# Optimization experiments

Hardware: AMD Instinct MI355X
Metric: run time of the kernel (lower is better)

The kernel has to match this reference:

```python
import jax, jax.numpy as jnp
import numpy as np

B, N, C, OUT, K2 = 64, 4096, 64, 64, 4  # batch, lattice sites, in/out features, kersize^2

def setup_inputs() -> dict:
    key = jax.random.key(0)
    k1, k2, k3, k4 = jax.random.split(key, 4)
    std = 0.5 / jnp.sqrt(K2 * (C + OUT))  # matches module's init stddev (W_scale=b_scale=1)
    x = jax.random.normal(k1, (B, N, C), dtype=jnp.float32)
    W = jax.random.normal(k2, (K2, C, OUT), dtype=jnp.float32) * std
    b = jax.random.normal(k3, (OUT,), dtype=jnp.float32) * std
    kernel2 = jax.random.randint(k4, (N, K2), 0, N, dtype=jnp.int32)
    return {"x": x, "W": W, "b": b, "kernel2": kernel2}

def reference(x, W, b, kernel2):
    # gather neighbors: [B, N, K2, C]; contract (K2, C) with W -> [B, N, OUT]
    y = jnp.einsum('bnkc,kco->bno', x[:, kernel2, :], W)
    # bias broadcast (original used tensordot with ones([B,N]))
    return y + b
```

## Files before the change

kernel.cpp:

```cpp
#include <hip/hip_runtime.h>
#include <stdint.h>


#define N_SITES  4096
#define C_DIM    64
#define OUT_DIM  64

typedef __attribute__((ext_vector_type(8))) short bf16x8;
typedef __attribute__((ext_vector_type(4))) float f32x4;

__device__ __forceinline__ uint32_t pack2_bf16(float f0, float f1) {
    uint32_t u0 = __float_as_uint(f0) + 0x8000u;
    uint32_t u1 = __float_as_uint(f1) + 0x8000u;
    return __builtin_amdgcn_perm(u1, u0, 0x07060302u);
}

template<int N> __device__ __forceinline__ void wait_vmcnt() {
    asm volatile("s_waitcnt vmcnt(%0)" :: "n"(N) : "memory");
}

__device__ __forceinline__ void gll16(const float* p, uint32_t m0v) {
    asm volatile("s_mov_b32 m0, %1\n\t"
                 "global_load_lds_dwordx4 %0, off"
                 :: "v"(p), "s"(m0v) : "memory");
}

__global__ __launch_bounds__(64, 1)
void conv_async_kernel(const float* __restrict__ x, const float* __restrict__ W,
                       const float* __restrict__ bias, const int* __restrict__ kernel2,
                       float* __restrict__ out)
{
    __shared__ __align__(16) uint8_t lds_raw[33792];

    const int lane = threadIdx.x;
    const int bi   = blockIdx.x;
    const int sg   = bi >> 4;
    const int bg   = bi & 15;
    const int n0   = sg * 64;
    const int b0   = bg * 4;

    const int c  = lane & 15;
    const int q  = lane >> 4;
    const int sl = c >> 2;
    const int bb = c & 3;

    {
        int4 iv = ((const int4*)kernel2)[n0 + lane];
        *(int4*)(lds_raw + 32768 + lane * 16) = iv;
    }

    bf16x8 aw[4][8];
    #pragma unroll
    for (int t = 0; t < 4; ++t)
        #pragma unroll
        for (int s = 0; s < 8; ++s) {
            uint32_t* ap = (uint32_t*)&aw[t][s];
            #pragma unroll
            for (int u = 0; u < 4; ++u) {
                float f0 = W[(size_t)(s*32 + q*8 + 2*u    ) * OUT_DIM + t*16 + c];
                float f1 = W[(size_t)(s*32 + q*8 + 2*u + 1) * OUT_DIM + t*16 + c];
                ap[u] = pack2_bf16(f0, f1);
            }
        }

    f32x4 bias_r[4];
    #pragma unroll
    for (int t = 0; t < 4; ++t) bias_r[t] = *(const f32x4*)&bias[t*16 + q*4];

    const float* gx = x + (size_t)(b0 + bb) * (N_SITES * C_DIM) + q * 4;

    const uint32_t lds0 =
        __builtin_amdgcn_readfirstlane((uint32_t)(uintptr_t)lds_raw);

    wait_vmcnt<0>();

    auto issue_tile = [&](int pp) {
        const uint8_t* ib = lds_raw + 32768 + pp * 64;
        int4 iv0 = *(const int4*)(ib);
        int4 iv1 = *(const int4*)(ib + 16);
        int4 iv2 = *(const int4*)(ib + 32);
        int4 iv3 = *(const int4*)(ib + 48);
        const uint32_t m0b = lds0 + (uint32_t)(pp & 1) * 16384;
        #pragma unroll
        for (int ks = 0; ks < 4; ++ks) {
            const int e0 = ks==0 ? iv0.x : ks==1 ? iv0.y : ks==2 ? iv0.z : iv0.w;
            const int e1 = ks==0 ? iv1.x : ks==1 ? iv1.y : ks==2 ? iv1.z : iv1.w;
            const int e2 = ks==0 ? iv2.x : ks==1 ? iv2.y : ks==2 ? iv2.z : iv2.w;
            const int e3 = ks==0 ? iv3.x : ks==1 ? iv3.y : ks==2 ? iv3.z : iv3.w;
            const int nk = (sl & 2) ? ((sl & 1) ? e3 : e2)
                                    : ((sl & 1) ? e1 : e0);
            const float* row = gx + (size_t)(uint32_t)nk * C_DIM;
            gll16(row,      m0b + (uint32_t)(ks*4 + 0) * 1024);
            gll16(row + 16, m0b + (uint32_t)(ks*4 + 1) * 1024);
            gll16(row + 32, m0b + (uint32_t)(ks*4 + 2) * 1024);
            gll16(row + 48, m0b + (uint32_t)(ks*4 + 3) * 1024);
        }
    };

    issue_tile(0);
    issue_tile(1);

    #pragma unroll
    for (int p = 0; p < 16; ++p) {
        if      (p == 0)  wait_vmcnt<16>();
        else if (p == 1)  wait_vmcnt<20>();
        else if (p == 15) wait_vmcnt<8>();
        else              wait_vmcnt<24>();

        const uint32_t tb = (uint32_t)(p & 1) * 16384;
        f32x4 acc[4];
        #pragma unroll
        for (int t = 0; t < 4; ++t) acc[t] = (f32x4){0.f, 0.f, 0.f, 0.f};

        #pragma unroll
        for (int s = 0; s < 8; ++s) {
            const uint8_t* pb = lds_raw + tb + s*2048 + q*512 + c*16;
            f32x4 xa = *(const f32x4*)(pb);
            f32x4 xb = *(const f32x4*)(pb + 256);
            bf16x8 bf;
            uint32_t* bp = (uint32_t*)&bf;
            bp[0] = pack2_bf16(xa[0], xa[1]);
            bp[1] = pack2_bf16(xa[2], xa[3]);
            bp[2] = pack2_bf16(xb[0], xb[1]);
            bp[3] = pack2_bf16(xb[2], xb[3]);
            #pragma unroll
            for (int t = 0; t < 4; ++t)
                acc[t] = __builtin_amdgcn_mfma_f32_16x16x32_bf16(aw[t][s], bf, acc[t], 0, 0, 0);
        }

        if (p + 2 < 16) issue_tile(p + 2);

        const int n = n0 + p*4 + sl;
        float* op = out + ((size_t)(b0 + bb) * N_SITES + n) * OUT_DIM + q*4;
        #pragma unroll
        for (int t = 0; t < 4; ++t)
            *(f32x4*)(op + t*16) = acc[t] + bias_r[t];
    }
}

extern "C" void kernel_launch(void* const* d_in, const int* in_sizes, int n_in,
                              void* d_out, int out_size, void* d_ws, size_t ws_size,
                              hipStream_t stream) {
    const float* x       = (const float*)d_in[0];
    const float* W       = (const float*)d_in[1];
    const float* bias    = (const float*)d_in[2];
    const int*   kernel2 = (const int*)d_in[3];
    float* out = (float*)d_out;

    conv_async_kernel<<<1024, 64, 0, stream>>>(x, W, bias, kernel2, out);
}
```

Measured before the change: 144.7 us.

## Halve per-block site tile and pipeline gathers in half-tiles to double grid

```diff
diff --git a/kernel.cpp b/kernel.cpp
--- a/kernel.cpp
+++ b/kernel.cpp
@@ -30,13 +30,13 @@
                        const float* __restrict__ bias, const int* __restrict__ kernel2,
                        float* __restrict__ out)
 {
-    __shared__ __align__(16) uint8_t lds_raw[33792];
+    __shared__ __align__(16) uint8_t lds_raw[16896];
 
     const int lane = threadIdx.x;
     const int bi   = blockIdx.x;
     const int sg   = bi >> 4;
     const int bg   = bi & 15;
-    const int n0   = sg * 64;
+    const int n0   = sg * 32;
     const int b0   = bg * 4;
 
     const int c  = lane & 15;
@@ -44,9 +44,9 @@
     const int sl = c >> 2;
     const int bb = c & 3;
 
-    {
+    if (lane < 32) {
         int4 iv = ((const int4*)kernel2)[n0 + lane];
-        *(int4*)(lds_raw + 32768 + lane * 16) = iv;
+        *(int4*)(lds_raw + 16384 + lane * 16) = iv;
     }
 
     bf16x8 aw[4][8];
@@ -74,46 +74,34 @@
 
     wait_vmcnt<0>();
 
-    auto issue_tile = [&](int pp) {
-        const uint8_t* ib = lds_raw + 32768 + pp * 64;
-        int4 iv0 = *(const int4*)(ib);
-        int4 iv1 = *(const int4*)(ib + 16);
-        int4 iv2 = *(const int4*)(ib + 32);
-        int4 iv3 = *(const int4*)(ib + 48);
-        const uint32_t m0b = lds0 + (uint32_t)(pp & 1) * 16384;
+    auto issue_ht = [&](int i) {
+        const uint8_t* ib = lds_raw + 16384 + (i >> 1) * 64 + (i & 1) * 8;
+        int2 iv0 = *(const int2*)(ib);
+        int2 iv1 = *(const int2*)(ib + 16);
+        int2 iv2 = *(const int2*)(ib + 32);
+        int2 iv3 = *(const int2*)(ib + 48);
+        const uint32_t m0b = lds0 + (uint32_t)(i & 1) * 8192;
         #pragma unroll
-        for (int ks = 0; ks < 4; ++ks) {
-            const int e0 = ks==0 ? iv0.x : ks==1 ? iv0.y : ks==2 ? iv0.z : iv0.w;
-            const int e1 = ks==0 ? iv1.x : ks==1 ? iv1.y : ks==2 ? iv1.z : iv1.w;
-            const int e2 = ks==0 ? iv2.x : ks==1 ? iv2.y : ks==2 ? iv2.z : iv2.w;
-            const int e3 = ks==0 ? iv3.x : ks==1 ? iv3.y : ks==2 ? iv3.z : iv3.w;
+        for (int kl = 0; kl < 2; ++kl) {
+            const int e0 = kl ? iv0.y : iv0.x;
+            const int e1 = kl ? iv1.y : iv1.x;
+            const int e2 = kl ? iv2.y : iv2.x;
+            const int e3 = kl ? iv3.y : iv3.x;
             const int nk = (sl & 2) ? ((sl & 1) ? e3 : e2)
                                     : ((sl & 1) ? e1 : e0);
             const float* row = gx + (size_t)(uint32_t)nk * C_DIM;
-            gll16(row,      m0b + (uint32_t)(ks*4 + 0) * 1024);
-            gll16(row + 16, m0b + (uint32_t)(ks*4 + 1) * 1024);
-            gll16(row + 32, m0b + (uint32_t)(ks*4 + 2) * 1024);
-            gll16(row + 48, m0b + (uint32_t)(ks*4 + 3) * 1024);
+            gll16(row,      m0b + (uint32_t)(kl*4 + 0) * 1024);
+            gll16(row + 16, m0b + (uint32_t)(kl*4 + 1) * 1024);
+            gll16(row + 32, m0b + (uint32_t)(kl*4 + 2) * 1024);
+            gll16(row + 48, m0b + (uint32_t)(kl*4 + 3) * 1024);
         }
     };
 
-    issue_tile(0);
-    issue_tile(1);
-
-    #pragma unroll
-    for (int p = 0; p < 16; ++p) {
-        if      (p == 0)  wait_vmcnt<16>();
-        else if (p == 1)  wait_vmcnt<20>();
-        else if (p == 15) wait_vmcnt<8>();
-        else              wait_vmcnt<24>();
-
-        const uint32_t tb = (uint32_t)(p & 1) * 16384;
-        f32x4 acc[4];
+    auto comp_ht = [&](int i, f32x4* acc) {
+        const uint32_t tb = (uint32_t)(i & 1) * 8192;
+        const int hb = (i & 1) * 4;
         #pragma unroll
-        for (int t = 0; t < 4; ++t) acc[t] = (f32x4){0.f, 0.f, 0.f, 0.f};
-
-        #pragma unroll
-        for (int s = 0; s < 8; ++s) {
+        for (int s = 0; s < 4; ++s) {
             const uint8_t* pb = lds_raw + tb + s*2048 + q*512 + c*16;
             f32x4 xa = *(const f32x4*)(pb);
             f32x4 xb = *(const f32x4*)(pb + 256);
@@ -125,10 +113,29 @@
             bp[3] = pack2_bf16(xb[2], xb[3]);
             #pragma unroll
             for (int t = 0; t < 4; ++t)
-                acc[t] = __builtin_amdgcn_mfma_f32_16x16x32_bf16(aw[t][s], bf, acc[t], 0, 0, 0);
+                acc[t] = __builtin_amdgcn_mfma_f32_16x16x32_bf16(aw[t][hb + s], bf, acc[t], 0, 0, 0);
         }
+    };
 
-        if (p + 2 < 16) issue_tile(p + 2);
+    issue_ht(0);
+    issue_ht(1);
+
+    #pragma unroll
+    for (int p = 0; p < 8; ++p) {
+        f32x4 acc[4];
+        #pragma unroll
+        for (int t = 0; t < 4; ++t) acc[t] = (f32x4){0.f, 0.f, 0.f, 0.f};
+
+        if (p == 0) wait_vmcnt<8>();
+        else        wait_vmcnt<12>();
+        comp_ht(2*p, acc);
+        if (p < 7) issue_ht(2*p + 2);
+
+        if      (p == 0) wait_vmcnt<8>();
+        else if (p == 7) wait_vmcnt<4>();
+        else             wait_vmcnt<12>();
+        comp_ht(2*p + 1, acc);
+        if (p < 7) issue_ht(2*p + 3);
 
         const int n = n0 + p*4 + sl;
         float* op = out + ((size_t)(b0 + bb) * N_SITES + n) * OUT_DIM + q*4;
@@ -147,5 +154,5 @@
     const int*   kernel2 = (const int*)d_in[3];
     float* out = (float*)d_out;
 
-    conv_async_kernel<<<1024, 64, 0, stream>>>(x, W, bias, kernel2, out);
+    conv_async_kernel<<<2048, 64, 0, stream>>>(x, W, bias, kernel2, out);
 }
```

New measurement: 149.8 us. 1.04x slower.

## Gather neighbor rows into registers with triple-buffered loads instead of LDS DMA

Applied to the files above, without the earlier changes.

```diff
diff --git a/kernel.cpp b/kernel.cpp
--- a/kernel.cpp
+++ b/kernel.cpp
@@ -19,24 +19,36 @@
     asm volatile("s_waitcnt vmcnt(%0)" :: "n"(N) : "memory");
 }
 
-__device__ __forceinline__ void gll16(const float* p, uint32_t m0v) {
-    asm volatile("s_mov_b32 m0, %1\n\t"
-                 "global_load_lds_dwordx4 %0, off"
-                 :: "v"(p), "s"(m0v) : "memory");
+template<int OFF>
+__device__ __forceinline__ void gld16(f32x4& d, const float* p) {
+    asm volatile("global_load_dwordx4 %0, %1, off offset:%2"
+                 : "=v"(d) : "v"(p), "n"(OFF) : "memory");
+}
+
+__host__ __device__ constexpr int wait_for(int i) {
+    return (i == 0 || i == 1) ? 16
+         : (i == 2)           ? 20
+         : (i == 14)          ? 16
+         : (i == 15)          ? 4
+         : (i & 1)            ? 20
+         : 24;
 }
 
 __global__ __launch_bounds__(64, 1)
-void conv_async_kernel(const float* __restrict__ x, const float* __restrict__ W,
-                       const float* __restrict__ bias, const int* __restrict__ kernel2,
-                       float* __restrict__ out)
+void conv_vgather_kernel(const float* __restrict__ x, const float* __restrict__ W,
+                         const float* __restrict__ bias, const int* __restrict__ kernel2,
+                         float* __restrict__ out)
 {
-    __shared__ __align__(16) uint8_t lds_raw[33792];
+    __shared__ __align__(16) int lds_idx[32 * 4];
 
     const int lane = threadIdx.x;
     const int bi   = blockIdx.x;
-    const int sg   = bi >> 4;
-    const int bg   = bi & 15;
-    const int n0   = sg * 64;
+    const int half = bi >> 10;
+    const int r    = bi & 1023;
+    const int bgl  = r & 7;
+    const int sg   = r >> 3;
+    const int bg   = bgl + half * 8;
+    const int n0   = sg * 32;
     const int b0   = bg * 4;
 
     const int c  = lane & 15;
@@ -44,10 +56,8 @@
     const int sl = c >> 2;
     const int bb = c & 3;
 
-    {
-        int4 iv = ((const int4*)kernel2)[n0 + lane];
-        *(int4*)(lds_raw + 32768 + lane * 16) = iv;
-    }
+    if (lane < 32)
+        ((int4*)lds_idx)[lane] = ((const int4*)kernel2)[n0 + lane];
 
     bf16x8 aw[4][8];
     #pragma unroll
@@ -67,75 +77,79 @@
     #pragma unroll
     for (int t = 0; t < 4; ++t) bias_r[t] = *(const f32x4*)&bias[t*16 + q*4];
 
-    const float* gx = x + (size_t)(b0 + bb) * (N_SITES * C_DIM) + q * 4;
-
-    const uint32_t lds0 =
-        __builtin_amdgcn_readfirstlane((uint32_t)(uintptr_t)lds_raw);
+    const float* gxb = x + (size_t)(b0 + bb) * (N_SITES * C_DIM) + q * 8;
 
     wait_vmcnt<0>();
+    __builtin_amdgcn_sched_barrier(0);
 
-    auto issue_tile = [&](int pp) {
-        const uint8_t* ib = lds_raw + 32768 + pp * 64;
-        int4 iv0 = *(const int4*)(ib);
-        int4 iv1 = *(const int4*)(ib + 16);
-        int4 iv2 = *(const int4*)(ib + 32);
-        int4 iv3 = *(const int4*)(ib + 48);
-        const uint32_t m0b = lds0 + (uint32_t)(pp & 1) * 16384;
-        #pragma unroll
-        for (int ks = 0; ks < 4; ++ks) {
-            const int e0 = ks==0 ? iv0.x : ks==1 ? iv0.y : ks==2 ? iv0.z : iv0.w;
-            const int e1 = ks==0 ? iv1.x : ks==1 ? iv1.y : ks==2 ? iv1.z : iv1.w;
-            const int e2 = ks==0 ? iv2.x : ks==1 ? iv2.y : ks==2 ? iv2.z : iv2.w;
-            const int e3 = ks==0 ? iv3.x : ks==1 ? iv3.y : ks==2 ? iv3.z : iv3.w;
-            const int nk = (sl & 2) ? ((sl & 1) ? e3 : e2)
-                                    : ((sl & 1) ? e1 : e0);
-            const float* row = gx + (size_t)(uint32_t)nk * C_DIM;
-            gll16(row,      m0b + (uint32_t)(ks*4 + 0) * 1024);
-            gll16(row + 16, m0b + (uint32_t)(ks*4 + 1) * 1024);
-            gll16(row + 32, m0b + (uint32_t)(ks*4 + 2) * 1024);
-            gll16(row + 48, m0b + (uint32_t)(ks*4 + 3) * 1024);
-        }
+    f32x4 buf0[8], buf1[8], buf2[8];
+
+    auto issue = [&](f32x4* buf, int i) {
+        const int2 tk = *(const int2*)&lds_idx[(i >> 1) * 16 + sl * 4 + (i & 1) * 2];
+        const float* p0 = gxb + (size_t)(uint32_t)tk.x * C_DIM;
+        const float* p1 = gxb + (size_t)(uint32_t)tk.y * C_DIM;
+        gld16<0>(buf[0], p0); gld16<16>(buf[1], p0);
+        gld16<128>(buf[2], p0); gld16<144>(buf[3], p0);
+        gld16<0>(buf[4], p1); gld16<16>(buf[5], p1);
+        gld16<128>(buf[6], p1); gld16<144>(buf[7], p1);
     };
 
-    issue_tile(0);
-    issue_tile(1);
+    auto comp = [&](const f32x4* buf, int h, f32x4* acc) {
+        #pragma unroll
+        for (int tl = 0; tl < 2; ++tl)
+            #pragma unroll
+            for (int hs = 0; hs < 2; ++hs) {
+                const f32x4 xa = buf[tl*4 + hs*2];
+                const f32x4 xb = buf[tl*4 + hs*2 + 1];
+                bf16x8 bf;
+                uint32_t* bp = (uint32_t*)&bf;
+                bp[0] = pack2_bf16(xa[0], xa[1]);
+                bp[1] = pack2_bf16(xa[2], xa[3]);
+                bp[2] = pack2_bf16(xb[0], xb[1]);
+                bp[3] = pack2_bf16(xb[2], xb[3]);
+                #pragma unroll
+                for (int t = 0; t < 4; ++t)
+                    acc[t] = __builtin_amdgcn_mfma_f32_16x16x32_bf16(
+                        aw[t][h*4 + tl*2 + hs], bf, acc[t], 0, 0, 0);
+            }
+    };
 
-    #pragma unroll
-    for (int p = 0; p < 16; ++p) {
-        if      (p == 0)  wait_vmcnt<16>();
-        else if (p == 1)  wait_vmcnt<20>();
-        else if (p == 15) wait_vmcnt<8>();
-        else              wait_vmcnt<24>();
-
-        const uint32_t tb = (uint32_t)(p & 1) * 16384;
-        f32x4 acc[4];
-        #pragma unroll
-        for (int t = 0; t < 4; ++t) acc[t] = (f32x4){0.f, 0.f, 0.f, 0.f};
-
-        #pragma unroll
-        for (int s = 0; s < 8; ++s) {
-            const uint8_t* pb = lds_raw + tb + s*2048 + q*512 + c*16;
-            f32x4 xa = *(const f32x4*)(pb);
-            f32x4 xb = *(const f32x4*)(pb + 256);
-            bf16x8 bf;
-            uint32_t* bp = (uint32_t*)&bf;
-            bp[0] = pack2_bf16(xa[0], xa[1]);
-            bp[1] = pack2_bf16(xa[2], xa[3]);
-            bp[2] = pack2_bf16(xb[0], xb[1]);
-            bp[3] = pack2_bf16(xb[2], xb[3]);
-            #pragma unroll
-            for (int t = 0; t < 4; ++t)
-                acc[t] = __builtin_amdgcn_mfma_f32_16x16x32_bf16(aw[t][s], bf, acc[t], 0, 0, 0);
-        }
-
-        if (p + 2 < 16) issue_tile(p + 2);
-
-        const int n = n0 + p*4 + sl;
-        float* op = out + ((size_t)(b0 + bb) * N_SITES + n) * OUT_DIM + q*4;
+    auto dostore = [&](int p, const f32x4* acc) {
+        const int n = n0 + p * 4 + sl;
+        float* op = out + ((size_t)(b0 + bb) * N_SITES + n) * OUT_DIM + q * 4;
         #pragma unroll
         for (int t = 0; t < 4; ++t)
             *(f32x4*)(op + t*16) = acc[t] + bias_r[t];
+    };
+
+    issue(buf0, 0);
+    issue(buf1, 1);
+    issue(buf2, 2);
+
+    f32x4 acc[4];
+
+    #define STEP(i)                                                           \
+    {                                                                         \
+        wait_vmcnt<wait_for(i)>();                                            \
+        __builtin_amdgcn_sched_barrier(0);                                    \
+        f32x4* bcur = ((i) % 3 == 0) ? buf0 : ((i) % 3 == 1) ? buf1 : buf2;   \
+        if (((i) & 1) == 0) {                                                 \
+            acc[0] = (f32x4){0.f,0.f,0.f,0.f};                                \
+            acc[1] = (f32x4){0.f,0.f,0.f,0.f};                                \
+            acc[2] = (f32x4){0.f,0.f,0.f,0.f};                                \
+            acc[3] = (f32x4){0.f,0.f,0.f,0.f};                                \
+        }                                                                     \
+        comp(bcur, (i) & 1, acc);                                             \
+        if ((i) <= 12) issue(bcur, (i) + 3);                                  \
+        if ((i) & 1) dostore((i) >> 1, acc);                                  \
     }
+
+    STEP(0);  STEP(1);  STEP(2);  STEP(3);
+    STEP(4);  STEP(5);  STEP(6);  STEP(7);
+    STEP(8);  STEP(9);  STEP(10); STEP(11);
+    STEP(12); STEP(13); STEP(14); STEP(15);
+
+    #undef STEP
 }
 
 extern "C" void kernel_launch(void* const* d_in, const int* in_sizes, int n_in,
@@ -147,5 +161,5 @@
     const int*   kernel2 = (const int*)d_in[3];
     float* out = (float*)d_out;
 
-    conv_async_kernel<<<1024, 64, 0, stream>>>(x, W, bias, kernel2, out);
+    conv_vgather_kernel<<<2048, 64, 0, stream>>>(x, W, bias, kernel2, out);
 }
```

Measured after the change: 146.0 us. Within noise of the previous version (+1.0%).
